# Optimization experiments

Measured on AMD Instinct MI355X. Metric: run time of the kernel, lower is better.

## Reference

```python
import jax, jax.numpy as jnp
import numpy as np

B, S, D, H = 8, 1024, 512, 12
HS = D // H  # 42 (head_size; 12*42 = 504 concat width, as in the original)


def setup_inputs() -> dict:
    key = jax.random.key(0)
    ks = jax.random.split(key, 12)
    sd = 0.02
    return {
        "embedded_patches": jax.random.normal(ks[0], (B, S, D), dtype=jnp.float32),
        # stacked per-head projections (12 independent Linear(D, HS, bias=False))
        "wk": jax.random.normal(ks[1], (H, D, HS), dtype=jnp.float32) * sd,
        "wq": jax.random.normal(ks[2], (H, D, HS), dtype=jnp.float32) * sd,
        "wv": jax.random.normal(ks[3], (H, D, HS), dtype=jnp.float32) * sd,
        "w_proj": jax.random.normal(ks[4], (H * HS, D), dtype=jnp.float32) * sd,  # [504, 512]
        "b_proj": jnp.zeros((D,), dtype=jnp.float32),
        # shared LayerNorm (same params used for both norms, as in the original)
        "gamma": jnp.ones((D,), dtype=jnp.float32),
        "beta": jnp.zeros((D,), dtype=jnp.float32),
        "w1": jax.random.normal(ks[5], (D, 4 * D), dtype=jnp.float32) * sd,
        "b1": jnp.zeros((4 * D,), dtype=jnp.float32),
        "w2": jax.random.normal(ks[6], (4 * D, D), dtype=jnp.float32) * sd,
        "b2": jnp.zeros((D,), dtype=jnp.float32),
    }


def _layernorm(x, gamma, beta, eps=1e-5):
    mu = jnp.mean(x, axis=-1, keepdims=True)
    var = jnp.var(x, axis=-1, keepdims=True)
    return (x - mu) * jax.lax.rsqrt(var + eps) * gamma + beta


def reference(embedded_patches, wk, wq, wv, w_proj, b_proj, gamma, beta, w1, b1, w2, b2):
    x = embedded_patches
    n1 = _layernorm(x, gamma, beta)
    # per-head projections, vectorized over heads: [B,S,D] x [H,D,E] -> [B,H,S,E]
    q = jnp.einsum('bsd,hde->bhse', n1, wq)
    k = jnp.einsum('bsd,hde->bhse', n1, wk)
    v = jnp.einsum('bsd,hde->bhse', n1, wv)
    scale = HS ** -0.5
    wei = jax.nn.softmax(jnp.einsum('bhse,bhte->bhst', q, k) * scale, axis=-1)
    out = jnp.einsum('bhst,bhte->bhse', wei, v)        # [B,H,S,E]
    out = out.transpose(0, 2, 1, 3).reshape(B, S, H * HS)  # concat heads -> [B,S,504]
    attn = out @ w_proj + b_proj                       # [B,S,D]
    # original quirk: takes batch element 0 and broadcasts against residual
    first_added = attn[0] + x                          # [S,D] + [B,S,D] -> [B,S,D]
    n2 = _layernorm(first_added, gamma, beta)
    h = jax.nn.gelu(n2 @ w1 + b1, approximate=False)   # torch nn.GELU default = exact erf
    ff = h @ w2 + b2
    return ff + first_added
```

## Files before the change

### kernel.cpp

```cpp
#include <hip/hip_runtime.h>
#include <hip/hip_bf16.h>
#include <stdint.h>


typedef unsigned short u16;
typedef __attribute__((ext_vector_type(8))) short short8;
typedef __attribute__((ext_vector_type(4))) float f32x4;

__device__ __forceinline__ u16 f2bf(float f) {
  union { float f; unsigned u; } x; x.f = f;
  return (u16)((x.u + 0x7FFFu + ((x.u >> 16) & 1u)) >> 16);
}
__device__ __forceinline__ float bf2f(u16 u) {
  union { unsigned u; float f; } x; x.u = ((unsigned)u) << 16;
  return x.f;
}

__device__ __forceinline__ void gload_lds16(const u16* g, u16* l) {
  __builtin_amdgcn_global_load_lds(
      (__attribute__((address_space(1))) void*)g,
      (__attribute__((address_space(3))) void*)l, 16, 0, 0);
}

__device__ __forceinline__ float wred_sum(float v) {
#pragma unroll
  for (int off = 32; off > 0; off >>= 1) v += __shfl_xor(v, off, 64);
  return v;
}

__device__ __forceinline__ float gelu_fast(float t) {
  const float p = __builtin_fmaf(0.0356774081f, t * t, 0.7978845608f);
  return t / (1.0f + __expf(-2.0f * t * p));
}

#define MFMA16x16(a, b, c) __builtin_amdgcn_mfma_f32_16x16x32_bf16(a, b, c, 0, 0, 0)

enum { EP_BF16 = 0, EP_F32B = 2, EP_GELU = 3, EP_ATOM = 7 };

template <int EP>
__launch_bounds__(256, 4)
__global__ void gemm2(const u16* __restrict__ A, int lda, long sAz,
                      const u16* __restrict__ Bt, int ldb, long sBz,
                      void* __restrict__ Cv, int ldc, long sCz,
                      int K, const float* __restrict__ bias) {
  __shared__ u16 lA[2][128 * 32];
  __shared__ u16 lB[2][128 * 32];

  const int gx = gridDim.x, gy = gridDim.y;
  const int lin = blockIdx.x + gx * (blockIdx.y + gy * blockIdx.z);
  const int nwg = gx * gy * gridDim.z;
  const int wg = (lin & 7) * (nwg >> 3) + (lin >> 3);
  const int bx = wg % gx;
  const int tmp = wg / gx;
  const int by = tmp % gy;
  const int z = tmp / gy;

  const u16* Ab = A + (long)z * sAz;
  const u16* Bb = Bt + (long)z * sBz;
  const int m0 = bx * 128;
  const int n0 = by * 128;
  const int tid = threadIdx.x;
  const int w = tid >> 6;
  const int l = tid & 63;
  const int wr = w >> 1;
  const int wc = w & 1;
  const int NT = K >> 5;

  f32x4 acc[4][4];
#pragma unroll
  for (int i = 0; i < 4; ++i)
#pragma unroll
    for (int j = 0; j < 4; ++j) acc[i][j] = (f32x4){0.f, 0.f, 0.f, 0.f};

  const int srow = w * 32 + (l >> 2);
  const int sk = (l & 3) * 8;
  const u16* ga0 = Ab + (long)(m0 + srow) * lda + sk;
  const u16* ga1 = Ab + (long)(m0 + srow + 16) * lda + sk;
  const u16* gb0 = Bb + (long)(n0 + srow) * ldb + sk;
  const u16* gb1 = Bb + (long)(n0 + srow + 16) * ldb + sk;
  const int dOff = w * 1024;

  const int aoff = (wr * 64 + (l & 15)) * 32 + (l >> 4) * 8;
  const int boff = (wc * 64 + (l & 15)) * 32 + (l >> 4) * 8;

  gload_lds16(ga0, &lA[0][dOff]);
  gload_lds16(ga1, &lA[0][dOff + 512]);
  gload_lds16(gb0, &lB[0][dOff]);
  gload_lds16(gb1, &lB[0][dOff + 512]);
  __syncthreads();

  int buf = 0;
  for (int t = 0; t < NT; ++t) {
    short8 af[4], bfv[4];
#pragma unroll
    for (int mi = 0; mi < 4; ++mi)
      af[mi] = *(const short8*)&lA[buf][aoff + mi * 16 * 32];
#pragma unroll
    for (int ni = 0; ni < 4; ++ni)
      bfv[ni] = *(const short8*)&lB[buf][boff + ni * 16 * 32];
    if (t + 1 < NT) {
      const int k0 = (t + 1) * 32;
      const int nb = buf ^ 1;
      gload_lds16(ga0 + k0, &lA[nb][dOff]);
      gload_lds16(ga1 + k0, &lA[nb][dOff + 512]);
      gload_lds16(gb0 + k0, &lB[nb][dOff]);
      gload_lds16(gb1 + k0, &lB[nb][dOff + 512]);
    }
#pragma unroll
    for (int mi = 0; mi < 4; ++mi)
#pragma unroll
      for (int ni = 0; ni < 4; ++ni)
        acc[mi][ni] = MFMA16x16(af[mi], bfv[ni], acc[mi][ni]);
    __syncthreads();
    buf ^= 1;
  }

  const int rbase = m0 + wr * 64 + (l >> 4) * 4;
  const int cbase = n0 + wc * 64 + (l & 15);
#pragma unroll
  for (int mi = 0; mi < 4; ++mi) {
#pragma unroll
    for (int ni = 0; ni < 4; ++ni) {
#pragma unroll
      for (int j = 0; j < 4; ++j) {
        const int row = rbase + mi * 16 + j;
        const int col = cbase + ni * 16;
        const float v = acc[mi][ni][j];
        if (EP == EP_BF16) {
          ((u16*)Cv)[(long)z * sCz + (long)row * ldc + col] = f2bf(v);
        } else if (EP == EP_F32B) {
          ((float*)Cv)[(long)row * ldc + col] = v + bias[col];
        } else if (EP == EP_GELU) {
          ((u16*)Cv)[(long)row * ldc + col] = f2bf(gelu_fast(v + bias[col]));
        } else {
          atomicAdd(&((float*)Cv)[(long)row * ldc + col], v);
        }
      }
    }
  }
}

__device__ __forceinline__ short8 frag_read(const u16* base, int row, int ks,
                                            int l) {
  const int g = (ks * 4 + (l >> 4)) ^ (l & 7);
  return *(const short8*)&base[row * 64 + g * 8];
}

__launch_bounds__(256, 2)
__global__ void flash_attn(const u16* __restrict__ qkvc,
                           const u16* __restrict__ vt,
                           u16* __restrict__ cat) {
  __shared__ u16 lQ[64 * 64];
  __shared__ u16 lK[2][64 * 64];
  __shared__ u16 lV[2][64 * 64];
  __shared__ u16 lP[4][16 * 64];
  const int h = blockIdx.x;
  const int q0 = blockIdx.y * 64;
  const int tid = threadIdx.x;
  const int w = tid >> 6;
  const int l = tid & 63;
  const int sg = ((l & 7) ^ (l >> 3)) * 8;
  const int sr = w * 8 + (l >> 3);

#define FA_STAGE(t_, b_)                                                    \
  do {                                                                      \
    const int kv_ = (t_) * 64;                                              \
    gload_lds16(qkvc + (long)(kv_ + sr) * 1536 + 768 + h * 64 + sg,         \
                lK[b_] + w * 8 * 64);                                       \
    gload_lds16(qkvc + (long)(kv_ + 32 + sr) * 1536 + 768 + h * 64 + sg,    \
                lK[b_] + (32 + w * 8) * 64);                                \
    gload_lds16(vt + (long)(h * 128 + sr) * 1024 + kv_ + sg,                \
                lV[b_] + w * 8 * 64);                                       \
    gload_lds16(vt + (long)(h * 128 + 32 + sr) * 1024 + kv_ + sg,           \
                lV[b_] + (32 + w * 8) * 64);                                \
  } while (0)

  gload_lds16(qkvc + (long)(q0 + sr) * 1536 + h * 64 + sg, lQ + w * 8 * 64);
  gload_lds16(qkvc + (long)(q0 + 32 + sr) * 1536 + h * 64 + sg,
              lQ + (32 + w * 8) * 64);
  FA_STAGE(0, 0);
  __syncthreads();

  const short8 qf0 = frag_read(lQ, w * 16 + (l & 15), 0, l);
  const short8 qf1 = frag_read(lQ, w * 16 + (l & 15), 1, l);

  f32x4 accO[4];
  float m_run[4], l_run[4];
#pragma unroll
  for (int i = 0; i < 4; ++i) {
    accO[i] = (f32x4){0.f, 0.f, 0.f, 0.f};
    m_run[i] = -3.0e38f;
    l_run[i] = 0.f;
  }

  int buf = 0;
  for (int t = 0; t < 16; ++t) {
    if (t + 1 < 16) FA_STAGE(t + 1, buf ^ 1);
    f32x4 s[4];
#pragma unroll
    for (int ni = 0; ni < 4; ++ni) {
      const short8 kf0 = frag_read(lK[buf], ni * 16 + (l & 15), 0, l);
      const short8 kf1 = frag_read(lK[buf], ni * 16 + (l & 15), 1, l);
      s[ni] = MFMA16x16(qf0, kf0, ((f32x4){0.f, 0.f, 0.f, 0.f}));
      s[ni] = MFMA16x16(qf1, kf1, s[ni]);
    }
#pragma unroll
    for (int j = 0; j < 4; ++j) {
      float mx = fmaxf(fmaxf(s[0][j], s[1][j]), fmaxf(s[2][j], s[3][j]));
      mx = fmaxf(mx, __shfl_xor(mx, 1));
      mx = fmaxf(mx, __shfl_xor(mx, 2));
      mx = fmaxf(mx, __shfl_xor(mx, 4));
      mx = fmaxf(mx, __shfl_xor(mx, 8));
      const float mn = fmaxf(m_run[j], mx);
      const float corr = __expf(m_run[j] - mn);
      m_run[j] = mn;
      float ps = 0.f;
#pragma unroll
      for (int ni = 0; ni < 4; ++ni) {
        const float p = __expf(s[ni][j] - mn);
        s[ni][j] = p;
        ps += p;
      }
      ps += __shfl_xor(ps, 1);
      ps += __shfl_xor(ps, 2);
      ps += __shfl_xor(ps, 4);
      ps += __shfl_xor(ps, 8);
      l_run[j] = l_run[j] * corr + ps;
#pragma unroll
      for (int ne = 0; ne < 4; ++ne) accO[ne][j] *= corr;
    }
#pragma unroll
    for (int ni = 0; ni < 4; ++ni) {
#pragma unroll
      for (int j = 0; j < 4; ++j) {
        const int row = (l >> 4) * 4 + j;
        const int col = ni * 16 + (l & 15);
        const int boff = row * 128 + (((col >> 3) ^ (row & 7)) << 4) +
                         (col & 7) * 2;
        *(u16*)((char*)lP[w] + boff) = f2bf(s[ni][j]);
      }
    }
    asm volatile("s_waitcnt lgkmcnt(0)" ::: "memory");
    __builtin_amdgcn_sched_barrier(0);
    const short8 pf0 = frag_read(lP[w], (l & 15), 0, l);
    const short8 pf1 = frag_read(lP[w], (l & 15), 1, l);
#pragma unroll
    for (int ne = 0; ne < 4; ++ne) {
      const short8 vf0 = frag_read(lV[buf], ne * 16 + (l & 15), 0, l);
      const short8 vf1 = frag_read(lV[buf], ne * 16 + (l & 15), 1, l);
      accO[ne] = MFMA16x16(pf0, vf0, accO[ne]);
      accO[ne] = MFMA16x16(pf1, vf1, accO[ne]);
    }
    __syncthreads();
    buf ^= 1;
  }
#undef FA_STAGE

#pragma unroll
  for (int j = 0; j < 4; ++j) {
    const float inv = 1.0f / l_run[j];
    const int row = q0 + w * 16 + (l >> 4) * 4 + j;
#pragma unroll
    for (int ne = 0; ne < 4; ++ne) {
      const int e = ne * 16 + (l & 15);
      if (e < 42)
        cat[(long)row * 512 + h * 42 + e] = f2bf(accO[ne][j] * inv);
    }
  }
}

__device__ __forceinline__ void transpose_body(const float* __restrict__ in,
                                               u16* __restrict__ out, int N,
                                               int Kin, int Kpad, int blk,
                                               int gx, int t, float* smem) {
  const int n0 = (blk % gx) * 64;
  const int k0 = (blk / gx) * 64;
  const int tc = t & 63;
  const int tr = t >> 6;
#pragma unroll
  for (int r = 0; r < 16; ++r) {
    const int kr = tr * 16 + r;
    const int kg = k0 + kr;
    smem[kr * 65 + tc] = (kg < Kin) ? in[(long)kg * N + n0 + tc] : 0.f;
  }
  __syncthreads();
  const int nr0 = t >> 4;
  const int kc = (t & 15) * 4;
#pragma unroll
  for (int p = 0; p < 4; ++p) {
    const int nr = nr0 + p * 16;
    ushort4 v;
    v.x = f2bf(smem[(kc + 0) * 65 + nr]);
    v.y = f2bf(smem[(kc + 1) * 65 + nr]);
    v.z = f2bf(smem[(kc + 2) * 65 + nr]);
    v.w = f2bf(smem[(kc + 3) * 65 + nr]);
    *(ushort4*)&out[(long)(n0 + nr) * Kpad + k0 + kc] = v;
  }
}

__device__ __forceinline__ float wredsum_lane(float v) {
#pragma unroll
  for (int off = 32; off > 0; off >>= 1) v += __shfl_xor(v, off, 64);
  return v;
}

__global__ void prep_fused(const float* __restrict__ wq,
                           const float* __restrict__ wk,
                           const float* __restrict__ wv,
                           const float* __restrict__ w_proj,
                           const float* __restrict__ w1,
                           const float* __restrict__ w2,
                           const float* __restrict__ x,
                           const float* __restrict__ gamma,
                           const float* __restrict__ beta,
                           u16* __restrict__ BtQKV, u16* __restrict__ wvT,
                           u16* __restrict__ BtP, u16* __restrict__ Bt1,
                           u16* __restrict__ Bt2, u16* __restrict__ cat,
                           u16* __restrict__ n1, float scale) {
  __shared__ float smem[64 * 65];
  const int blk = blockIdx.x;
  const int t = threadIdx.x;
  if (blk < 3072) {
    const int i = blk * 256 + t;
    const int n = i >> 9, d = i & 511;
    const int pq = n / 768;
    const int h = (n % 768) >> 6;
    const int e = n & 63;
    float v = 0.f;
    if (e < 42) {
      v = (pq ? wk : wq)[((long)h * 512 + d) * 42 + e];
      if (!pq) v *= scale;
    }
    BtQKV[i] = f2bf(v);
  } else if (blk < 6144) {
    const int i = (blk - 3072) * 256 + t;
    const int r = i >> 9, d = i & 511;
    const int h = r >> 7, e = r & 127;
    wvT[i] = f2bf(e < 42 ? wv[((long)h * 512 + d) * 42 + e] : 0.f);
  } else if (blk < 6208) {
    transpose_body(w_proj, BtP, 512, 504, 512, blk - 6144, 8, t, smem);
  } else if (blk < 6464) {
    transpose_body(w1, Bt1, 2048, 512, 512, blk - 6208, 32, t, smem);
  } else if (blk < 6720) {
    transpose_body(w2, Bt2, 512, 2048, 2048, blk - 6464, 8, t, smem);
  } else if (blk < 8768) {
    cat[(blk - 6720) * 256 + t] = 0;
  } else {
    const int s = blk - 8768;
    const float* row = x + (long)s * 512;
    const float v0 = row[t];
    const float v1 = row[t + 256];
    float sum = wredsum_lane(v0 + v1);
    float sq = wredsum_lane(v0 * v0 + v1 * v1);
    if ((t & 63) == 0) { smem[t >> 6] = sum; smem[8 + (t >> 6)] = sq; }
    __syncthreads();
    sum = smem[0] + smem[1] + smem[2] + smem[3];
    sq = smem[8] + smem[9] + smem[10] + smem[11];
    const float mu = sum * (1.0f / 512.0f);
    const float rstd = rsqrtf(sq * (1.0f / 512.0f) - mu * mu + 1e-5f);
    n1[(long)s * 512 + t] = f2bf((v0 - mu) * rstd * gamma[t] + beta[t]);
    n1[(long)s * 512 + t + 256] =
        f2bf((v1 - mu) * rstd * gamma[t + 256] + beta[t + 256]);
  }
}

__global__ void ln2_kernel(const float* __restrict__ x,
                           const float* __restrict__ aproj,
                           const float* __restrict__ gamma,
                           const float* __restrict__ beta,
                           const float* __restrict__ b2,
                           u16* __restrict__ n2, float* __restrict__ outp) {
  __shared__ float red[16];
  const int r = blockIdx.x;
  const int t = threadIdx.x;
  const int s = r & 1023;
  const float* xr = x + (long)r * 512;
  const float* ar = aproj + (long)s * 512;
  const float v0 = xr[t] + ar[t];
  const float v1 = xr[t + 256] + ar[t + 256];
  outp[(long)r * 512 + t] = v0 + b2[t];
  outp[(long)r * 512 + t + 256] = v1 + b2[t + 256];
  float sum = wred_sum(v0 + v1);
  float sq = wred_sum(v0 * v0 + v1 * v1);
  if ((t & 63) == 0) { red[t >> 6] = sum; red[8 + (t >> 6)] = sq; }
  __syncthreads();
  sum = red[0] + red[1] + red[2] + red[3];
  sq = red[8] + red[9] + red[10] + red[11];
  const float mu = sum * (1.0f / 512.0f);
  const float rstd = rsqrtf(sq * (1.0f / 512.0f) - mu * mu + 1e-5f);
  n2[(long)r * 512 + t] = f2bf((v0 - mu) * rstd * gamma[t] + beta[t]);
  n2[(long)r * 512 + t + 256] =
      f2bf((v1 - mu) * rstd * gamma[t + 256] + beta[t + 256]);
}

extern "C" void kernel_launch(void* const* d_in, const int* in_sizes, int n_in,
                              void* d_out, int out_size, void* d_ws,
                              size_t ws_size, hipStream_t stream) {
  const float* x = (const float*)d_in[0];
  const float* wk = (const float*)d_in[1];
  const float* wq = (const float*)d_in[2];
  const float* wv = (const float*)d_in[3];
  const float* w_proj = (const float*)d_in[4];
  const float* b_proj = (const float*)d_in[5];
  const float* gamma = (const float*)d_in[6];
  const float* beta = (const float*)d_in[7];
  const float* w1 = (const float*)d_in[8];
  const float* b1 = (const float*)d_in[9];
  const float* w2 = (const float*)d_in[10];
  const float* b2 = (const float*)d_in[11];

  char* base = (char*)d_ws;
  size_t off = 0;
  auto alloc = [&](size_t bytes) -> void* {
    void* p = base + off;
    off += (bytes + 255) & ~(size_t)255;
    return p;
  };
  u16* n1 = (u16*)alloc(1024L * 512 * 2);
  u16* qkvc = (u16*)alloc(1024L * 1536 * 2);
  u16* wvT = (u16*)alloc(1536L * 512 * 2);
  u16* vt = (u16*)alloc(1536L * 1024 * 2);
  u16* cat = (u16*)alloc(1024L * 512 * 2);
  float* aproj = (float*)alloc(1024L * 512 * 4);
  u16* n2 = (u16*)alloc(8192L * 512 * 2);
  u16* hbuf = (u16*)alloc(8192L * 2048 * 2);
  u16* BtQKV = (u16*)alloc(1536L * 512 * 2);
  u16* BtP = (u16*)alloc(512L * 512 * 2);
  u16* Bt1 = (u16*)alloc(2048L * 512 * 2);
  u16* Bt2 = (u16*)alloc(512L * 2048 * 2);
  (void)ws_size; (void)in_sizes; (void)n_in; (void)out_size;

  const float scale = 0.15430334996209191f;

  prep_fused<<<9792, 256, 0, stream>>>(wq, wk, wv, w_proj, w1, w2, x, gamma,
                                       beta, BtQKV, wvT, BtP, Bt1, Bt2, cat,
                                       n1, scale);

  gemm2<EP_BF16><<<dim3(8, 12, 1), 256, 0, stream>>>(
      n1, 512, 0, BtQKV, 512, 0, qkvc, 1536, 0, 512, nullptr);
  gemm2<EP_BF16><<<dim3(12, 8, 1), 256, 0, stream>>>(
      wvT, 512, 0, n1, 512, 0, vt, 1024, 0, 512, nullptr);
  flash_attn<<<dim3(12, 16), 256, 0, stream>>>(qkvc, vt, cat);
  gemm2<EP_F32B><<<dim3(8, 4, 1), 256, 0, stream>>>(
      cat, 512, 0, BtP, 512, 0, aproj, 512, 0, 512, b_proj);
  ln2_kernel<<<8192, 256, 0, stream>>>(x, aproj, gamma, beta, b2, n2,
                                       (float*)d_out);
  gemm2<EP_GELU><<<dim3(64, 16, 1), 256, 0, stream>>>(
      n2, 512, 0, Bt1, 512, 0, hbuf, 2048, 0, 512, b1);
  gemm2<EP_ATOM><<<dim3(64, 4, 2), 256, 0, stream>>>(
      hbuf, 2048, 1024, Bt2, 2048, 1024, d_out, 512, 0, 1024, nullptr);
}
```

Before: 165.2 us.

## Templatize GEMM on BK, merge QKV and V^T GEMMs, remap tile order

Moves the GEMM body into a device function templated on the K-tile depth. The final FFN down-projection now uses BK=64, which halves the barrier and loop count per K step at the cost of more LDS and lower occupancy. The QKV and V-transpose GEMMs are merged into a single 192-block launch, removing one launch and letting both run concurrently. The workgroup-to-tile mapping also changes so that consecutive swizzled groups walk the N dimension first, which alters cache reuse.

```diff
diff --git a/kernel.cpp b/kernel.cpp
--- a/kernel.cpp
+++ b/kernel.cpp
@@ -37,34 +37,26 @@
 
 enum { EP_BF16 = 0, EP_F32B = 2, EP_GELU = 3, EP_ATOM = 7 };
 
-template <int EP>
-__launch_bounds__(256, 4)
-__global__ void gemm2(const u16* __restrict__ A, int lda, long sAz,
-                      const u16* __restrict__ Bt, int ldb, long sBz,
-                      void* __restrict__ Cv, int ldc, long sCz,
-                      int K, const float* __restrict__ bias) {
-  __shared__ u16 lA[2][128 * 32];
-  __shared__ u16 lB[2][128 * 32];
-
-  const int gx = gridDim.x, gy = gridDim.y;
-  const int lin = blockIdx.x + gx * (blockIdx.y + gy * blockIdx.z);
-  const int nwg = gx * gy * gridDim.z;
-  const int wg = (lin & 7) * (nwg >> 3) + (lin >> 3);
-  const int bx = wg % gx;
-  const int tmp = wg / gx;
-  const int by = tmp % gy;
-  const int z = tmp / gy;
-
-  const u16* Ab = A + (long)z * sAz;
-  const u16* Bb = Bt + (long)z * sBz;
-  const int m0 = bx * 128;
-  const int n0 = by * 128;
+template <int EP, int BK>
+__device__ __forceinline__ void gemm_core(u16* lds, const u16* __restrict__ Ab,
+                                          int lda, const u16* __restrict__ Bb,
+                                          int ldb, void* __restrict__ Cv,
+                                          int ldc, int K,
+                                          const float* __restrict__ bias,
+                                          int m0, int n0) {
+  constexpr int GPR = BK / 8;
+  constexpr int RPI = 64 / GPR;
+  constexpr int IPM = 32 / RPI;
+  constexpr int TSZ = 128 * BK;
+  u16* lA[2] = {lds, lds + TSZ};
+  u16* lB[2] = {lds + 2 * TSZ, lds + 3 * TSZ};
+
   const int tid = threadIdx.x;
   const int w = tid >> 6;
   const int l = tid & 63;
   const int wr = w >> 1;
   const int wc = w & 1;
-  const int NT = K >> 5;
+  const int NT = K / BK;
 
   f32x4 acc[4][4];
 #pragma unroll
@@ -72,45 +64,46 @@
 #pragma unroll
     for (int j = 0; j < 4; ++j) acc[i][j] = (f32x4){0.f, 0.f, 0.f, 0.f};
 
-  const int srow = w * 32 + (l >> 2);
-  const int sk = (l & 3) * 8;
-  const u16* ga0 = Ab + (long)(m0 + srow) * lda + sk;
-  const u16* ga1 = Ab + (long)(m0 + srow + 16) * lda + sk;
-  const u16* gb0 = Bb + (long)(n0 + srow) * ldb + sk;
-  const u16* gb1 = Bb + (long)(n0 + srow + 16) * ldb + sk;
-  const int dOff = w * 1024;
-
-  const int aoff = (wr * 64 + (l & 15)) * 32 + (l >> 4) * 8;
-  const int boff = (wc * 64 + (l & 15)) * 32 + (l >> 4) * 8;
-
-  gload_lds16(ga0, &lA[0][dOff]);
-  gload_lds16(ga1, &lA[0][dOff + 512]);
-  gload_lds16(gb0, &lB[0][dOff]);
-  gload_lds16(gb1, &lB[0][dOff + 512]);
+  const int srow = w * 32 + l / GPR;
+  const int sk = (l % GPR) * 8;
+  const u16* gA = Ab + (long)(m0 + srow) * lda + sk;
+  const u16* gB = Bb + (long)(n0 + srow) * ldb + sk;
+  const int dOff = w * 32 * BK;
+
+  const int aoff = (wr * 64 + (l & 15)) * BK + (l >> 4) * 8;
+  const int boff = (wc * 64 + (l & 15)) * BK + (l >> 4) * 8;
+
+  auto stage = [&](int b_, int t_) {
+#pragma unroll
+    for (int i = 0; i < IPM; ++i) {
+      gload_lds16(gA + (long)t_ * BK + (long)i * RPI * lda,
+                  lA[b_] + dOff + i * RPI * BK);
+      gload_lds16(gB + (long)t_ * BK + (long)i * RPI * ldb,
+                  lB[b_] + dOff + i * RPI * BK);
+    }
+  };
+
+  stage(0, 0);
   __syncthreads();
 
   int buf = 0;
   for (int t = 0; t < NT; ++t) {
-    short8 af[4], bfv[4];
-#pragma unroll
-    for (int mi = 0; mi < 4; ++mi)
-      af[mi] = *(const short8*)&lA[buf][aoff + mi * 16 * 32];
-#pragma unroll
-    for (int ni = 0; ni < 4; ++ni)
-      bfv[ni] = *(const short8*)&lB[buf][boff + ni * 16 * 32];
-    if (t + 1 < NT) {
-      const int k0 = (t + 1) * 32;
-      const int nb = buf ^ 1;
-      gload_lds16(ga0 + k0, &lA[nb][dOff]);
-      gload_lds16(ga1 + k0, &lA[nb][dOff + 512]);
-      gload_lds16(gb0 + k0, &lB[nb][dOff]);
-      gload_lds16(gb1 + k0, &lB[nb][dOff + 512]);
-    }
-#pragma unroll
-    for (int mi = 0; mi < 4; ++mi)
+    if (t + 1 < NT) stage(buf ^ 1, t + 1);
+#pragma unroll
+    for (int ks = 0; ks < BK / 32; ++ks) {
+      short8 af[4], bfv[4];
+#pragma unroll
+      for (int mi = 0; mi < 4; ++mi)
+        af[mi] = *(const short8*)&lA[buf][aoff + mi * 16 * BK + ks * 32];
 #pragma unroll
       for (int ni = 0; ni < 4; ++ni)
-        acc[mi][ni] = MFMA16x16(af[mi], bfv[ni], acc[mi][ni]);
+        bfv[ni] = *(const short8*)&lB[buf][boff + ni * 16 * BK + ks * 32];
+#pragma unroll
+      for (int mi = 0; mi < 4; ++mi)
+#pragma unroll
+        for (int ni = 0; ni < 4; ++ni)
+          acc[mi][ni] = MFMA16x16(af[mi], bfv[ni], acc[mi][ni]);
+    }
     __syncthreads();
     buf ^= 1;
   }
@@ -127,7 +120,7 @@
         const int col = cbase + ni * 16;
         const float v = acc[mi][ni][j];
         if (EP == EP_BF16) {
-          ((u16*)Cv)[(long)z * sCz + (long)row * ldc + col] = f2bf(v);
+          ((u16*)Cv)[(long)row * ldc + col] = f2bf(v);
         } else if (EP == EP_F32B) {
           ((float*)Cv)[(long)row * ldc + col] = v + bias[col];
         } else if (EP == EP_GELU) {
@@ -137,6 +130,46 @@
         }
       }
     }
+  }
+}
+
+template <int EP, int BK>
+__launch_bounds__(256, (BK == 32 ? 4 : 2))
+__global__ void gemm_k(const u16* __restrict__ A, int lda, long sAz,
+                       const u16* __restrict__ Bt, int ldb, long sBz,
+                       void* __restrict__ Cv, int ldc, int K,
+                       const float* __restrict__ bias) {
+  __shared__ u16 lds[4 * 128 * BK];
+  const int gx = gridDim.x, gy = gridDim.y, gz = gridDim.z;
+  const int lin = blockIdx.x + gx * (blockIdx.y + gy * blockIdx.z);
+  const int nwg = gx * gy * gz;
+  const int wg = (lin & 7) * (nwg >> 3) + (lin >> 3);
+  const int by = wg % gy;
+  const int rem = wg / gy;
+  const int z = rem % gz;
+  const int bx = rem / gz;
+  const u16* Ab = A + (long)z * sAz;
+  const u16* Bb = Bt + (long)z * sBz;
+  gemm_core<EP, BK>(lds, Ab, lda, Bb, ldb, Cv, ldc, K, bias, bx * 128,
+                    by * 128);
+}
+
+__launch_bounds__(256, 4)
+__global__ void qkvt_kernel(const u16* __restrict__ n1,
+                            const u16* __restrict__ BtQKV,
+                            u16* __restrict__ qkvc,
+                            const u16* __restrict__ wvT,
+                            u16* __restrict__ vt) {
+  __shared__ u16 lds[4 * 128 * 32];
+  const int lin = blockIdx.x;
+  const int wg = (lin & 7) * 24 + (lin >> 3);
+  if (wg < 96) {
+    gemm_core<EP_BF16, 32>(lds, n1, 512, BtQKV, 512, qkvc, 1536, 512, nullptr,
+                           (wg & 7) * 128, (wg >> 3) * 128);
+  } else {
+    const int v = wg - 96;
+    gemm_core<EP_BF16, 32>(lds, wvT, 512, n1, 512, vt, 1024, 512, nullptr,
+                           (v % 12) * 128, (v / 12) * 128);
   }
 }
 
@@ -296,12 +329,6 @@
     v.w = f2bf(smem[(kc + 3) * 65 + nr]);
     *(ushort4*)&out[(long)(n0 + nr) * Kpad + k0 + kc] = v;
   }
-}
-
-__device__ __forceinline__ float wredsum_lane(float v) {
-#pragma unroll
-  for (int off = 32; off > 0; off >>= 1) v += __shfl_xor(v, off, 64);
-  return v;
 }
 
 __global__ void prep_fused(const float* __restrict__ wq,
@@ -350,8 +377,8 @@
     const float* row = x + (long)s * 512;
     const float v0 = row[t];
     const float v1 = row[t + 256];
-    float sum = wredsum_lane(v0 + v1);
-    float sq = wredsum_lane(v0 * v0 + v1 * v1);
+    float sum = wred_sum(v0 + v1);
+    float sq = wred_sum(v0 * v0 + v1 * v1);
     if ((t & 63) == 0) { smem[t >> 6] = sum; smem[8 + (t >> 6)] = sq; }
     __syncthreads();
     sum = smem[0] + smem[1] + smem[2] + smem[3];
@@ -435,18 +462,14 @@
   prep_fused<<<9792, 256, 0, stream>>>(wq, wk, wv, w_proj, w1, w2, x, gamma,
                                        beta, BtQKV, wvT, BtP, Bt1, Bt2, cat,
                                        n1, scale);
-
-  gemm2<EP_BF16><<<dim3(8, 12, 1), 256, 0, stream>>>(
-      n1, 512, 0, BtQKV, 512, 0, qkvc, 1536, 0, 512, nullptr);
-  gemm2<EP_BF16><<<dim3(12, 8, 1), 256, 0, stream>>>(
-      wvT, 512, 0, n1, 512, 0, vt, 1024, 0, 512, nullptr);
+  qkvt_kernel<<<192, 256, 0, stream>>>(n1, BtQKV, qkvc, wvT, vt);
   flash_attn<<<dim3(12, 16), 256, 0, stream>>>(qkvc, vt, cat);
-  gemm2<EP_F32B><<<dim3(8, 4, 1), 256, 0, stream>>>(
-      cat, 512, 0, BtP, 512, 0, aproj, 512, 0, 512, b_proj);
+  gemm_k<EP_F32B, 32><<<dim3(8, 4, 1), 256, 0, stream>>>(
+      cat, 512, 0, BtP, 512, 0, aproj, 512, 512, b_proj);
   ln2_kernel<<<8192, 256, 0, stream>>>(x, aproj, gamma, beta, b2, n2,
                                        (float*)d_out);
-  gemm2<EP_GELU><<<dim3(64, 16, 1), 256, 0, stream>>>(
-      n2, 512, 0, Bt1, 512, 0, hbuf, 2048, 0, 512, b1);
-  gemm2<EP_ATOM><<<dim3(64, 4, 2), 256, 0, stream>>>(
-      hbuf, 2048, 1024, Bt2, 2048, 1024, d_out, 512, 0, 1024, nullptr);
-}
+  gemm_k<EP_GELU, 32><<<dim3(64, 16, 1), 256, 0, stream>>>(
+      n2, 512, 0, Bt1, 512, 0, hbuf, 2048, 512, b1);
+  gemm_k<EP_ATOM, 64><<<dim3(64, 4, 2), 256, 0, stream>>>(
+      hbuf, 2048, 1024, Bt2, 2048, 1024, d_out, 512, 1024, nullptr);
+}
```

New measurement: 158.1 us. 4.3% less time.
